# Performance work log

Hardware: AMD Instinct MI355X
Metric: run time of the kernel (lower is better)

## Reference

```python
import jax, jax.numpy as jnp
import numpy as np

N_NODES = 100000
N_EDGES = 1600000
IN_F = 128
HID = 128
OUT_F = 40


def _gcn_conv(x, W, b, src, dst):
    # PyG GCNConv: h = x @ W; out[dst] += norm * h[src]; out += b
    n = x.shape[0]
    h = x @ W  # [N, out_channels]
    deg = jnp.zeros((n,), h.dtype).at[dst].add(jnp.ones((dst.shape[0],), h.dtype))
    dinv = jnp.where(deg > 0, jax.lax.rsqrt(deg), 0.0)  # deg^{-1/2}
    norm = dinv[src] * dinv[dst]  # [E+N]
    msg = h[src] * norm[:, None]  # [E+N, out_channels] gather
    out = jnp.zeros_like(h).at[dst].add(msg)  # scatter-add at targets
    if b is not None:
        out = out + b
    return out


def setup_inputs() -> dict:
    key = jax.random.key(0)
    k_x, k_e, k1, k2, k3, kb1, kb2 = jax.random.split(key, 7)
    x = jax.random.normal(k_x, (N_NODES, IN_F), dtype=jnp.float32)
    edge_index = jax.random.randint(k_e, (2, N_EDGES), 0, N_NODES, dtype=jnp.int64)
    s_in = 1.0 / np.sqrt(IN_F)
    s_h = 1.0 / np.sqrt(HID)
    W_in = jax.random.normal(k1, (IN_F, HID), dtype=jnp.float32) * s_in
    b_in = jnp.zeros((HID,), dtype=jnp.float32)
    W_mid = jax.random.normal(k2, (HID, HID), dtype=jnp.float32) * s_h
    b_mid = jnp.zeros((HID,), dtype=jnp.float32)
    W_out = jax.random.normal(k3, (HID, OUT_F), dtype=jnp.float32) * s_h
    return {"x": x, "edge_index": edge_index, "W_in": W_in, "b_in": b_in,
            "W_mid": W_mid, "b_mid": b_mid, "W_out": W_out}


def reference(x, edge_index, W_in, b_in, W_mid, b_mid, W_out):
    n = x.shape[0]
    loops = jnp.arange(n, dtype=edge_index.dtype)
    src = jnp.concatenate([edge_index[0], loops])  # add self-loops
    dst = jnp.concatenate([edge_index[1], loops])
    h = jax.nn.relu(_gcn_conv(x, W_in, b_in, src, dst))
    h = jax.nn.relu(_gcn_conv(h, W_mid, b_mid, src, dst))
    h = _gcn_conv(h, W_out, None, src, dst)  # out_conv: bias=False
    return jax.nn.log_softmax(h, axis=1)
```

## Files before the change

### kernel.cpp

```cpp
#include <hip/hip_runtime.h>
#include <math.h>

#define N_NODES 100000
#define N_EDGES 1600000
#define NBUCK 391
#define BSTRIDE 4608

typedef __attribute__((ext_vector_type(8))) _Float16 h8v;
typedef __attribute__((ext_vector_type(4))) float f32x4;


__launch_bounds__(256)
__global__ void k_bpart(const int* __restrict__ srcv, const int* __restrict__ dstv,
                        int* __restrict__ bcnt, unsigned int* __restrict__ ebuf) {
    __shared__ int hist[NBUCK];
    __shared__ int cur[NBUCK];
    const int tid = threadIdx.x;
    for (int t = tid; t < NBUCK; t += 256) hist[t] = 0;
    __syncthreads();
    const int base = blockIdx.x * 4096;
#pragma unroll
    for (int i = 0; i < 16; i++) {
        int e = base + i * 256 + tid;
        if (e < N_EDGES) atomicAdd(&hist[dstv[e] >> 8], 1);
    }
    __syncthreads();
    for (int t = tid; t < NBUCK; t += 256)
        if (hist[t]) cur[t] = t * BSTRIDE + atomicAdd(&bcnt[t], hist[t]);
    __syncthreads();
#pragma unroll
    for (int i = 0; i < 16; i++) {
        int e = base + i * 256 + tid;
        if (e < N_EDGES) {
            int d = dstv[e];
            int p = atomicAdd(&cur[d >> 8], 1);
            ebuf[p] = ((unsigned int)srcv[e] << 8) | (unsigned int)(d & 255);
        }
    }
}

__launch_bounds__(256)
__global__ void k_bucket(const unsigned int* __restrict__ ebuf, const int* __restrict__ bcnt,
                         int2* __restrict__ rowse, float* __restrict__ dinv,
                         int* __restrict__ colidx) {
    __shared__ int cnt[256];
    __shared__ int s[256];
    __shared__ int cur[256];
    const int tid = threadIdx.x;
    const int b = blockIdx.x;
    const int e0 = b * BSTRIDE;
    const int e1 = e0 + bcnt[b];
    cnt[tid] = 0;
    __syncthreads();
    for (int e = e0 + tid; e < e1; e += 256) atomicAdd(&cnt[ebuf[e] & 255u], 1);
    __syncthreads();
    int v = cnt[tid];
    int x = v;
    s[tid] = x;
    __syncthreads();
    for (int d = 1; d < 256; d <<= 1) {
        int t = (tid >= d) ? s[tid - d] : 0;
        __syncthreads();
        x += t;
        s[tid] = x;
        __syncthreads();
    }
    int start = e0 + x - v;
    int node = b * 256 + tid;
    if (node < N_NODES) {
        rowse[node] = make_int2(start, start + v);
        dinv[node] = rsqrtf((float)(v + 1));
    }
    cur[tid] = start;
    __syncthreads();
    for (int e = e0 + tid; e < e1; e += 256) {
        unsigned int sd = ebuf[e];
        int pos = atomicAdd(&cur[sd & 255u], 1);
        colidx[pos] = (int)(sd >> 8);
    }
}

__global__ void k_zrows(_Float16* __restrict__ bufA, _Float16* __restrict__ zbuf) {
    int t = threadIdx.x;
    if (t < 128) bufA[(size_t)N_NODES * 128 + t] = (_Float16)0.f;
    if (t < 64)  zbuf[(size_t)N_NODES * 64 + t] = (_Float16)0.f;
}


__global__ void k_wprep_all(const float* __restrict__ W1, const float* __restrict__ W2,
                            const float* __restrict__ W3, _Float16* __restrict__ Wt) {
    int idx = blockIdx.x * blockDim.x + threadIdx.x;
    if (idx >= 304 * 128) return;
    int n = idx / 128, k = idx % 128;
    const float* W;
    int ncols, nloc;
    _Float16 *ph, *pl;
    if (n < 128)      { W = W1; ncols = 128; nloc = n;       ph = Wt;                 pl = Wt + 128 * 128; }
    else if (n < 256) { W = W2; ncols = 128; nloc = n - 128; ph = Wt + 2 * 128 * 128; pl = Wt + 3 * 128 * 128; }
    else              { W = W3; ncols = 40;  nloc = n - 256; ph = Wt + 4 * 128 * 128; pl = Wt + 4 * 128 * 128 + 48 * 128; }
    float v = (nloc < ncols) ? W[k * ncols + nloc] : 0.f;
    _Float16 hi = (_Float16)v;
    _Float16 lo = (_Float16)(v - (float)hi);
    ph[nloc * 128 + k] = hi;
    pl[nloc * 128 + k] = lo;
}


#define GEMM_GRID 625
#define NTILES 3125

__launch_bounds__(256, 2)
__global__ void k_gemm128_f32(const float* __restrict__ Af,
                              const _Float16* __restrict__ Wthi, const _Float16* __restrict__ Wtlo,
                              const float* __restrict__ dinv, _Float16* __restrict__ out) {
    const int lane = threadIdx.x & 63;
    const int wi = threadIdx.x >> 6;
    const int nb = wi * 32;
    const int nn = lane & 15;
    const int kq = (lane >> 4) * 8;
    const int quad = lane >> 4;

    h8v bh[4][2], bl[4][2];
#pragma unroll
    for (int c = 0; c < 4; c++)
#pragma unroll
        for (int t = 0; t < 2; t++) {
            int off = (nb + t * 16 + nn) * 128 + c * 32 + kq;
            bh[c][t] = *(const h8v*)(Wthi + off);
            bl[c][t] = *(const h8v*)(Wtlo + off);
        }

    for (int rt = blockIdx.x; rt < NTILES; rt += GEMM_GRID) {
        const int r0 = rt * 32;
        f32x4 acc[2][2] = {};
#pragma unroll
        for (int c = 0; c < 4; c++) {
            h8v a[2];
#pragma unroll
            for (int m = 0; m < 2; m++) {
                const float* p = Af + (size_t)(r0 + m * 16 + nn) * 128 + c * 32 + kq;
                float4 p0 = *(const float4*)p;
                float4 p1 = *(const float4*)(p + 4);
                h8v av = {(_Float16)p0.x, (_Float16)p0.y, (_Float16)p0.z, (_Float16)p0.w,
                          (_Float16)p1.x, (_Float16)p1.y, (_Float16)p1.z, (_Float16)p1.w};
                a[m] = av;
            }
#pragma unroll
            for (int m = 0; m < 2; m++)
#pragma unroll
                for (int t = 0; t < 2; t++) {
                    acc[m][t] = __builtin_amdgcn_mfma_f32_16x16x32_f16(a[m], bh[c][t], acc[m][t], 0, 0, 0);
                    acc[m][t] = __builtin_amdgcn_mfma_f32_16x16x32_f16(a[m], bl[c][t], acc[m][t], 0, 0, 0);
                }
        }
#pragma unroll
        for (int m = 0; m < 2; m++)
#pragma unroll
            for (int reg = 0; reg < 4; reg++) {
                int r = r0 + m * 16 + quad * 4 + reg;
                float dv = dinv[r];
#pragma unroll
                for (int t = 0; t < 2; t++)
                    out[(size_t)r * 128 + nb + t * 16 + nn] = (_Float16)(acc[m][t][reg] * dv);
            }
    }
}

__launch_bounds__(256, 2)
__global__ void k_gemm128(const _Float16* __restrict__ A,
                          const _Float16* __restrict__ Wthi, const _Float16* __restrict__ Wtlo,
                          const float* __restrict__ dinv, _Float16* __restrict__ out) {
    const int lane = threadIdx.x & 63;
    const int wi = threadIdx.x >> 6;
    const int nb = wi * 32;
    const int nn = lane & 15;
    const int kq = (lane >> 4) * 8;
    const int quad = lane >> 4;

    h8v bh[4][2], bl[4][2];
#pragma unroll
    for (int c = 0; c < 4; c++)
#pragma unroll
        for (int t = 0; t < 2; t++) {
            int off = (nb + t * 16 + nn) * 128 + c * 32 + kq;
            bh[c][t] = *(const h8v*)(Wthi + off);
            bl[c][t] = *(const h8v*)(Wtlo + off);
        }

    for (int rt = blockIdx.x; rt < NTILES; rt += GEMM_GRID) {
        const int r0 = rt * 32;
        f32x4 acc[2][2] = {};
#pragma unroll
        for (int c = 0; c < 4; c++) {
            h8v a[2];
#pragma unroll
            for (int m = 0; m < 2; m++)
                a[m] = *(const h8v*)(A + (size_t)(r0 + m * 16 + nn) * 128 + c * 32 + kq);
#pragma unroll
            for (int m = 0; m < 2; m++)
#pragma unroll
                for (int t = 0; t < 2; t++) {
                    acc[m][t] = __builtin_amdgcn_mfma_f32_16x16x32_f16(a[m], bh[c][t], acc[m][t], 0, 0, 0);
                    acc[m][t] = __builtin_amdgcn_mfma_f32_16x16x32_f16(a[m], bl[c][t], acc[m][t], 0, 0, 0);
                }
        }
#pragma unroll
        for (int m = 0; m < 2; m++)
#pragma unroll
            for (int reg = 0; reg < 4; reg++) {
                int r = r0 + m * 16 + quad * 4 + reg;
                float dv = dinv[r];
#pragma unroll
                for (int t = 0; t < 2; t++)
                    out[(size_t)r * 128 + nb + t * 16 + nn] = (_Float16)(acc[m][t][reg] * dv);
            }
    }
}

#define G40_GRID 160

__launch_bounds__(256, 2)
__global__ void k_gemm40(const _Float16* __restrict__ A,
                         const _Float16* __restrict__ Wthi, const _Float16* __restrict__ Wtlo,
                         const float* __restrict__ dinv, _Float16* __restrict__ out) {
    const int lane = threadIdx.x & 63;
    const int wi = threadIdx.x >> 6;
    const int nn = lane & 15;
    const int kq = (lane >> 4) * 8;
    const int quad = lane >> 4;

    h8v bh[4][3], bl[4][3];
#pragma unroll
    for (int c = 0; c < 4; c++)
#pragma unroll
        for (int t = 0; t < 3; t++) {
            int off = (t * 16 + nn) * 128 + c * 32 + kq;
            bh[c][t] = *(const h8v*)(Wthi + off);
            bl[c][t] = *(const h8v*)(Wtlo + off);
        }

    for (int rt = blockIdx.x * 4 + wi; rt < NTILES; rt += G40_GRID * 4) {
        const int r0 = rt * 32;
        f32x4 acc[2][3] = {};
#pragma unroll
        for (int c = 0; c < 4; c++) {
            h8v a[2];
#pragma unroll
            for (int m = 0; m < 2; m++)
                a[m] = *(const h8v*)(A + (size_t)(r0 + m * 16 + nn) * 128 + c * 32 + kq);
#pragma unroll
            for (int m = 0; m < 2; m++)
#pragma unroll
                for (int t = 0; t < 3; t++) {
                    acc[m][t] = __builtin_amdgcn_mfma_f32_16x16x32_f16(a[m], bh[c][t], acc[m][t], 0, 0, 0);
                    acc[m][t] = __builtin_amdgcn_mfma_f32_16x16x32_f16(a[m], bl[c][t], acc[m][t], 0, 0, 0);
                }
        }
#pragma unroll
        for (int m = 0; m < 2; m++)
#pragma unroll
            for (int reg = 0; reg < 4; reg++) {
                int r = r0 + m * 16 + quad * 4 + reg;
                float dv = dinv[r];
#pragma unroll
                for (int t = 0; t < 3; t++)
                    out[(size_t)r * 64 + t * 16 + nn] = (_Float16)(acc[m][t][reg] * dv);
            }
    }
}


__launch_bounds__(256)
__global__ void k_agg4(const _Float16* __restrict__ hp, const int2* __restrict__ rowse,
                       const int* __restrict__ colidx, const float* __restrict__ bias,
                       _Float16* __restrict__ outp) {
    const int lane = threadIdx.x & 63;
    const int wid = (blockIdx.x * blockDim.x + threadIdx.x) >> 6;
    const int rs = lane >> 4;
    const int cp = lane & 15;
    const int r = wid * 4 + rs;

    const int2 se = rowse[r];
    const int deg = se.y - se.x;
    int m = deg;
    m = max(m, __shfl_xor(m, 16));
    m = max(m, __shfl_xor(m, 32));

    const _Float16* hpc = hp + cp * 8;
    h8v acc = {};
    for (int it = 0; it < m; it += 4) {
        int i0 = se.x + it;
        int s0 = colidx[i0];
        int s1 = colidx[i0 + 1];
        int s2 = colidx[i0 + 2];
        int s3 = colidx[i0 + 3];
        s0 = (it < deg) ? s0 : N_NODES;
        s1 = (it + 1 < deg) ? s1 : N_NODES;
        s2 = (it + 2 < deg) ? s2 : N_NODES;
        s3 = (it + 3 < deg) ? s3 : N_NODES;
        h8v v0 = *(const h8v*)(hpc + (size_t)s0 * 128);
        h8v v1 = *(const h8v*)(hpc + (size_t)s1 * 128);
        h8v v2 = *(const h8v*)(hpc + (size_t)s2 * 128);
        h8v v3 = *(const h8v*)(hpc + (size_t)s3 * 128);
        acc += v0;
        acc += v1;
        acc += v2;
        acc += v3;
    }

    h8v sv = *(const h8v*)(hpc + (size_t)r * 128);
    float dv = rsqrtf((float)(deg + 1));
    const float* bp = bias + cp * 8;
    float4 b0 = *(const float4*)bp;
    float4 b1 = *(const float4*)(bp + 4);
    float bb[8] = {b0.x, b0.y, b0.z, b0.w, b1.x, b1.y, b1.z, b1.w};
    h8v o;
#pragma unroll
    for (int j = 0; j < 8; j++) {
        float s = (float)acc[j] + (float)sv[j];
        o[j] = (_Float16)fmaxf(fmaf(dv, s, bb[j]), 0.f);
    }
    *(h8v*)(outp + (size_t)r * 128 + cp * 8) = o;
}


__launch_bounds__(256)
__global__ void k_agg_out(const _Float16* __restrict__ hp, const int2* __restrict__ rowse,
                          const int* __restrict__ colidx, float* __restrict__ out) {
    const int lane = threadIdx.x & 63;
    const int wid = (blockIdx.x * blockDim.x + threadIdx.x) >> 6;
    const int rs = lane >> 3;
    const int cp = lane & 7;
    const int r = wid * 8 + rs;

    const int2 se = rowse[r];
    const int deg = se.y - se.x;
    int m = deg;
    m = max(m, __shfl_xor(m, 8));
    m = max(m, __shfl_xor(m, 16));
    m = max(m, __shfl_xor(m, 32));

    const _Float16* hpc = hp + cp * 8;
    h8v acc = {};
    for (int it = 0; it < m; it += 4) {
        int i0 = se.x + it;
        int s0 = colidx[i0];
        int s1 = colidx[i0 + 1];
        int s2 = colidx[i0 + 2];
        int s3 = colidx[i0 + 3];
        s0 = (it < deg) ? s0 : N_NODES;
        s1 = (it + 1 < deg) ? s1 : N_NODES;
        s2 = (it + 2 < deg) ? s2 : N_NODES;
        s3 = (it + 3 < deg) ? s3 : N_NODES;
        h8v v0 = *(const h8v*)(hpc + (size_t)s0 * 64);
        h8v v1 = *(const h8v*)(hpc + (size_t)s1 * 64);
        h8v v2 = *(const h8v*)(hpc + (size_t)s2 * 64);
        h8v v3 = *(const h8v*)(hpc + (size_t)s3 * 64);
        acc += v0;
        acc += v1;
        acc += v2;
        acc += v3;
    }

    h8v sv = *(const h8v*)(hpc + (size_t)r * 64);
    float dv = rsqrtf((float)(deg + 1));
    float z[8];
#pragma unroll
    for (int j = 0; j < 8; j++) z[j] = dv * ((float)acc[j] + (float)sv[j]);

    const bool act = cp < 5;
    float pm = -INFINITY;
    if (act) {
#pragma unroll
        for (int j = 0; j < 8; j++) pm = fmaxf(pm, z[j]);
    }
    pm = fmaxf(pm, __shfl_xor(pm, 1));
    pm = fmaxf(pm, __shfl_xor(pm, 2));
    pm = fmaxf(pm, __shfl_xor(pm, 4));
    float pe = 0.f;
    if (act) {
#pragma unroll
        for (int j = 0; j < 8; j++) pe += __expf(z[j] - pm);
    }
    pe += __shfl_xor(pe, 1);
    pe += __shfl_xor(pe, 2);
    pe += __shfl_xor(pe, 4);
    float lse = __logf(pe);
    if (act) {
        float* po = out + (size_t)r * 40 + cp * 8;
        float4 o0 = make_float4(z[0] - pm - lse, z[1] - pm - lse, z[2] - pm - lse, z[3] - pm - lse);
        float4 o1 = make_float4(z[4] - pm - lse, z[5] - pm - lse, z[6] - pm - lse, z[7] - pm - lse);
        *(float4*)po = o0;
        *(float4*)(po + 4) = o1;
    }
}


extern "C" void kernel_launch(void* const* d_in, const int* in_sizes, int n_in,
                              void* d_out, int out_size, void* d_ws, size_t ws_size,
                              hipStream_t stream) {
    const float* x     = (const float*)d_in[0];
    const int*   ei    = (const int*)d_in[1];
    const float* W_in  = (const float*)d_in[2];
    const float* b_in  = (const float*)d_in[3];
    const float* W_mid = (const float*)d_in[4];
    const float* b_mid = (const float*)d_in[5];
    const float* W_out = (const float*)d_in[6];
    float* out = (float*)d_out;

    const int* srcv = ei;
    const int* dstv = ei + N_EDGES;

    char* w = (char*)d_ws;
    float* dinv   = (float*)(w);
    int2* rowse   = (int2*)(w + (1ull << 19));
    int* bcnt     = (int*)(w + 1507328);
    int* colidx   = (int*)(w + (2ull << 20));
    unsigned int* ebuf = (unsigned int*)(w + (10ull << 20));
    _Float16* Wt  = (_Float16*)(w + (18ull << 20));
    _Float16* bufA = (_Float16*)(w + (19ull << 20));
    _Float16* bufB = (_Float16*)(w + (45ull << 20));
    _Float16* zbuf = (_Float16*)(w + (71ull << 20));

    _Float16* W1h = Wt;
    _Float16* W1l = Wt + 128 * 128;
    _Float16* W2h = Wt + 2 * 128 * 128;
    _Float16* W2l = Wt + 3 * 128 * 128;
    _Float16* W3h = Wt + 4 * 128 * 128;
    _Float16* W3l = Wt + 4 * 128 * 128 + 48 * 128;

    const int NB_PART = (N_EDGES + 4095) / 4096;

    hipMemsetAsync(bcnt, 0, NBUCK * sizeof(int), stream);
    k_zrows<<<1, 256, 0, stream>>>(bufA, zbuf);
    k_bpart<<<NB_PART, 256, 0, stream>>>(srcv, dstv, bcnt, ebuf);
    k_bucket<<<NBUCK, 256, 0, stream>>>(ebuf, bcnt, rowse, dinv, colidx);

    k_wprep_all<<<(304 * 128 + 255) / 256, 256, 0, stream>>>(W_in, W_mid, W_out, Wt);

    const int AGG4_BLOCKS = N_NODES / 16;
    const int AGGO_BLOCKS = N_NODES / 32;

    k_gemm128_f32<<<GEMM_GRID, 256, 0, stream>>>(x, W1h, W1l, dinv, bufA);
    k_agg4<<<AGG4_BLOCKS, 256, 0, stream>>>(bufA, rowse, colidx, b_in, bufB);
    k_gemm128<<<GEMM_GRID, 256, 0, stream>>>(bufB, W2h, W2l, dinv, bufA);
    k_agg4<<<AGG4_BLOCKS, 256, 0, stream>>>(bufA, rowse, colidx, b_mid, bufB);
    k_gemm40<<<G40_GRID, 256, 0, stream>>>(bufB, W3h, W3l, dinv, zbuf);
    k_agg_out<<<AGGO_BLOCKS, 256, 0, stream>>>(zbuf, rowse, colidx, out);
}
```

Before: 367.7 us.

## Store layer-1 features in column-sliced layout and aggregate per 16-column chunk

After: 400.2 us. 1.09x slower.

```diff
diff --git a/kernel.cpp b/kernel.cpp
--- a/kernel.cpp
+++ b/kernel.cpp
@@ -5,8 +5,10 @@
 #define N_EDGES 1600000
 #define NBUCK 391
 #define BSTRIDE 4608
+#define CSLICE ((N_NODES + 1) * 16)
 
 typedef __attribute__((ext_vector_type(8))) _Float16 h8v;
+typedef __attribute__((ext_vector_type(2))) _Float16 h2v;
 typedef __attribute__((ext_vector_type(4))) float f32x4;
 
 
@@ -80,8 +82,10 @@
     }
 }
 
-__global__ void k_zrows(_Float16* __restrict__ bufA, _Float16* __restrict__ zbuf) {
+__global__ void k_zrows(_Float16* __restrict__ bufC, _Float16* __restrict__ bufA,
+                        _Float16* __restrict__ zbuf) {
     int t = threadIdx.x;
+    if (t < 128) bufC[(size_t)(t >> 4) * CSLICE + (size_t)N_NODES * 16 + (t & 15)] = (_Float16)0.f;
     if (t < 128) bufA[(size_t)N_NODES * 128 + t] = (_Float16)0.f;
     if (t < 64)  zbuf[(size_t)N_NODES * 64 + t] = (_Float16)0.f;
 }
@@ -161,7 +165,8 @@
                 float dv = dinv[r];
 #pragma unroll
                 for (int t = 0; t < 2; t++)
-                    out[(size_t)r * 128 + nb + t * 16 + nn] = (_Float16)(acc[m][t][reg] * dv);
+                    out[(size_t)(wi * 2 + t) * CSLICE + (size_t)r * 16 + nn] =
+                        (_Float16)(acc[m][t][reg] * dv);
             }
     }
 }
@@ -267,6 +272,57 @@
                     out[(size_t)r * 64 + t * 16 + nn] = (_Float16)(acc[m][t][reg] * dv);
             }
     }
+}
+
+
+__launch_bounds__(256)
+__global__ void k_aggc(const _Float16* __restrict__ hp, const int2* __restrict__ rowse,
+                       const int* __restrict__ colidx, const float* __restrict__ bias,
+                       _Float16* __restrict__ outp) {
+    const int lane = threadIdx.x & 63;
+    const int wv = threadIdx.x >> 6;
+    const int chunk = blockIdx.x & 7;
+    const int rb = blockIdx.x >> 3;
+    const int rs = lane >> 3;
+    const int cp = lane & 7;
+    const int r = rb * 32 + wv * 8 + rs;
+
+    const int2 se = rowse[r];
+    const int deg = se.y - se.x;
+    int m = deg;
+    m = max(m, __shfl_xor(m, 8));
+    m = max(m, __shfl_xor(m, 16));
+    m = max(m, __shfl_xor(m, 32));
+
+    const _Float16* base = hp + (size_t)chunk * CSLICE + cp * 2;
+    h2v acc = {};
+    for (int it = 0; it < m; it += 4) {
+        int i0 = se.x + it;
+        int s0 = colidx[i0];
+        int s1 = colidx[i0 + 1];
+        int s2 = colidx[i0 + 2];
+        int s3 = colidx[i0 + 3];
+        s0 = (it < deg) ? s0 : N_NODES;
+        s1 = (it + 1 < deg) ? s1 : N_NODES;
+        s2 = (it + 2 < deg) ? s2 : N_NODES;
+        s3 = (it + 3 < deg) ? s3 : N_NODES;
+        h2v v0 = *(const h2v*)(base + (size_t)s0 * 16);
+        h2v v1 = *(const h2v*)(base + (size_t)s1 * 16);
+        h2v v2 = *(const h2v*)(base + (size_t)s2 * 16);
+        h2v v3 = *(const h2v*)(base + (size_t)s3 * 16);
+        acc += v0;
+        acc += v1;
+        acc += v2;
+        acc += v3;
+    }
+
+    h2v sv = *(const h2v*)(base + (size_t)r * 16);
+    float dv = rsqrtf((float)(deg + 1));
+    float2 b = *(const float2*)(bias + chunk * 16 + cp * 2);
+    float ox = fmaxf(fmaf(dv, (float)acc.x + (float)sv.x, b.x), 0.f);
+    float oy = fmaxf(fmaf(dv, (float)acc.y + (float)sv.y, b.y), 0.f);
+    h2v o = {(_Float16)ox, (_Float16)oy};
+    *(h2v*)(outp + (size_t)r * 128 + chunk * 16 + cp * 2) = o;
 }
 
 
@@ -421,6 +477,7 @@
     _Float16* bufA = (_Float16*)(w + (19ull << 20));
     _Float16* bufB = (_Float16*)(w + (45ull << 20));
     _Float16* zbuf = (_Float16*)(w + (71ull << 20));
+    _Float16* bufC = (_Float16*)(w + (84ull << 20));
 
     _Float16* W1h = Wt;
     _Float16* W1l = Wt + 128 * 128;
@@ -432,17 +489,18 @@
     const int NB_PART = (N_EDGES + 4095) / 4096;
 
     hipMemsetAsync(bcnt, 0, NBUCK * sizeof(int), stream);
-    k_zrows<<<1, 256, 0, stream>>>(bufA, zbuf);
+    k_zrows<<<1, 256, 0, stream>>>(bufC, bufA, zbuf);
     k_bpart<<<NB_PART, 256, 0, stream>>>(srcv, dstv, bcnt, ebuf);
     k_bucket<<<NBUCK, 256, 0, stream>>>(ebuf, bcnt, rowse, dinv, colidx);
 
     k_wprep_all<<<(304 * 128 + 255) / 256, 256, 0, stream>>>(W_in, W_mid, W_out, Wt);
 
+    const int AGGC_BLOCKS = 8 * (N_NODES / 32);
     const int AGG4_BLOCKS = N_NODES / 16;
     const int AGGO_BLOCKS = N_NODES / 32;
 
-    k_gemm128_f32<<<GEMM_GRID, 256, 0, stream>>>(x, W1h, W1l, dinv, bufA);
-    k_agg4<<<AGG4_BLOCKS, 256, 0, stream>>>(bufA, rowse, colidx, b_in, bufB);
+    k_gemm128_f32<<<GEMM_GRID, 256, 0, stream>>>(x, W1h, W1l, dinv, bufC);
+    k_aggc<<<AGGC_BLOCKS, 256, 0, stream>>>(bufC, rowse, colidx, b_in, bufB);
     k_gemm128<<<GEMM_GRID, 256, 0, stream>>>(bufB, W2h, W2l, dinv, bufA);
     k_agg4<<<AGG4_BLOCKS, 256, 0, stream>>>(bufA, rowse, colidx, b_mid, bufB);
     k_gemm40<<<G40_GRID, 256, 0, stream>>>(bufB, W3h, W3l, dinv, zbuf);
```
